# Kernel tuning notes

Measured on AMD Instinct MI355X. Metric: run time of the kernel, lower is better.

The kernel has to match this reference:

```python
import jax, jax.numpy as jnp
import numpy as np


def _igd(x, pf):
    # pf: [M, d] reference front, x: [N, d] candidate set
    # squared Euclidean distances via ||a||^2 + ||b||^2 - 2 a.b (cdist expansion)
    pf_sq = jnp.sum(pf * pf, axis=1, keepdims=True)          # [M, 1]
    x_sq = jnp.sum(x * x, axis=1, keepdims=True).T            # [1, N]
    cross = pf @ x.T                                          # [M, N]
    d2 = jnp.maximum(pf_sq + x_sq - 2.0 * cross, 0.0)
    dist = jnp.sqrt(d2)                                       # [M, N]
    # IGD: mean over reference points of min distance to candidate set
    return jnp.mean(jnp.min(dist, axis=1))


def setup_inputs() -> dict:
    key = jax.random.key(0)
    k1, k2 = jax.random.split(key)
    N, M, D = 16384, 16384, 64
    x = jax.random.normal(k1, (N, D), dtype=jnp.float32)
    pf = jax.random.normal(k2, (M, D), dtype=jnp.float32)
    return {"x": x, "pf": pf}


def reference(x, pf):
    return _igd(x, pf)
```

## Files before the change

kernel.cpp:

```cpp
#include <hip/hip_runtime.h>
#include <hip/hip_bf16.h>


typedef __bf16 bf16x8 __attribute__((ext_vector_type(8)));
typedef float f32x16 __attribute__((ext_vector_type(16)));

#define DIM 64
#define NSPLIT 12
#define MTILE 256

__global__ void pack_kernel(const float* __restrict__ x, const float* __restrict__ pf,
                            __bf16* __restrict__ Bp, __bf16* __restrict__ Ab,
                            float* __restrict__ xsq, float* __restrict__ pfsq,
                            float* __restrict__ out, int N, int M) {
    int gid = blockIdx.x * blockDim.x + threadIdx.x;
    if (gid == 0) out[0] = 0.f;
    if (gid < N * 4) {
        int col = gid >> 2, kf = gid & 3;
        const float* s = x + (size_t)col * DIM + kf * 16;
        float partial = 0.f;
        bf16x8 outv[2];
#pragma unroll
        for (int h = 0; h < 2; ++h) {
            float4 v0 = *(const float4*)(s + h * 8);
            float4 v1 = *(const float4*)(s + h * 8 + 4);
            float f[8] = {v0.x, v0.y, v0.z, v0.w, v1.x, v1.y, v1.z, v1.w};
#pragma unroll
            for (int i = 0; i < 8; ++i) {
                __bf16 b = (__bf16)f[i];
                outv[h][i] = b;
                float bb = (float)b;
                partial += bb * bb;
            }
        }
        int u = col >> 5, c31 = col & 31;
        *(bf16x8*)(Bp + ((size_t)(u * 4 + kf) * 64 + c31) * 8)      = outv[0];
        *(bf16x8*)(Bp + ((size_t)(u * 4 + kf) * 64 + 32 + c31) * 8) = outv[1];
        partial += __shfl_xor(partial, 1);
        partial += __shfl_xor(partial, 2);
        if (kf == 0) xsq[col] = partial;
    } else {
        int g = gid - N * 4;
        int row = g >> 2, q = g & 3;
        if (row >= M) return;
        const float* s = pf + (size_t)row * DIM + q * 16;
        float partial = 0.f;
        bf16x8 outv[2];
#pragma unroll
        for (int h = 0; h < 2; ++h) {
            float4 v0 = *(const float4*)(s + h * 8);
            float4 v1 = *(const float4*)(s + h * 8 + 4);
            float f[8] = {v0.x, v0.y, v0.z, v0.w, v1.x, v1.y, v1.z, v1.w};
#pragma unroll
            for (int i = 0; i < 8; ++i) {
                __bf16 b = (__bf16)(f[i] * -2.f);
                outv[h][i] = b;
                float bb = (float)b;
                partial += bb * bb;
            }
        }
        *(bf16x8*)(Ab + (size_t)row * DIM + q * 16)     = outv[0];
        *(bf16x8*)(Ab + (size_t)row * DIM + q * 16 + 8) = outv[1];
        partial += __shfl_xor(partial, 1);
        partial += __shfl_xor(partial, 2);
        if (q == 0) pfsq[row] = partial * 0.25f;
    }
}

__global__ __launch_bounds__(256, 3)
void igd_main(const __bf16* __restrict__ A, const __bf16* __restrict__ Bp,
              const float* __restrict__ xsq, float* __restrict__ partial, int N) {
    const int mTile  = blockIdx.x;
    const int nsplit = blockIdx.y;
    const int lane = threadIdx.x & 63;
    const int wave = threadIdx.x >> 6;
    const int half = lane >> 5;
    const int l31  = lane & 31;
    const int rowBase = mTile * MTILE + wave * 64;

    const int utotal = N / 32;
    const int ubase  = utotal / NSPLIT;
    const int urem   = utotal % NSPLIT;
    const int ustart = nsplit * ubase + (nsplit < urem ? nsplit : urem);
    const int ucount = ubase + (nsplit < urem ? 1 : 0);

    bf16x8 a[2][4];
#pragma unroll
    for (int g = 0; g < 2; ++g) {
        const __bf16* ap = A + (size_t)(rowBase + 32 * g + l31) * DIM + half * 8;
#pragma unroll
        for (int kf = 0; kf < 4; ++kf)
            a[g][kf] = *(const bf16x8*)(ap + kf * 16);
    }

    f32x16 zero, m0, m1;
#pragma unroll
    for (int r = 0; r < 16; ++r) { zero[r] = 0.f; m0[r] = 1e30f; m1[r] = 1e30f; }

    const __bf16* bbase = Bp + (size_t)ustart * 2048 + (size_t)lane * 8;
    const float*  xbase = xsq + ustart * 32 + l31;

    bf16x8 bA[4], bB[4];
    float xqA, xqB;

#define LOADU(breg, xq, u)                                                     \
    {                                                                          \
        const __bf16* p = bbase + (size_t)(u) * 2048;                          \
        breg[0] = *(const bf16x8*)(p);                                         \
        breg[1] = *(const bf16x8*)(p + 512);                                   \
        breg[2] = *(const bf16x8*)(p + 1024);                                  \
        breg[3] = *(const bf16x8*)(p + 1536);                                  \
        xq = xbase[(u) * 32];                                                  \
    }

#define COMPUTE(breg, xq)                                                      \
    {                                                                          \
        f32x16 acc0 = __builtin_amdgcn_mfma_f32_32x32x16_bf16(a[0][0], breg[0], zero, 0, 0, 0); \
        f32x16 acc1 = __builtin_amdgcn_mfma_f32_32x32x16_bf16(a[1][0], breg[0], zero, 0, 0, 0); \
        _Pragma("unroll")                                                      \
        for (int kf = 1; kf < 4; ++kf) {                                       \
            acc0 = __builtin_amdgcn_mfma_f32_32x32x16_bf16(a[0][kf], breg[kf], acc0, 0, 0, 0); \
            acc1 = __builtin_amdgcn_mfma_f32_32x32x16_bf16(a[1][kf], breg[kf], acc1, 0, 0, 0); \
        }                                                                      \
        _Pragma("unroll")                                                      \
        for (int r = 0; r < 16; ++r) {                                         \
            m0[r] = fminf(m0[r], acc0[r] + xq);                                \
            m1[r] = fminf(m1[r], acc1[r] + xq);                                \
        }                                                                      \
    }

    LOADU(bA, xqA, 0);
    int u = 0;
    for (; u + 2 < ucount; u += 2) {
        LOADU(bB, xqB, u + 1);
        COMPUTE(bA, xqA);
        LOADU(bA, xqA, u + 2);
        COMPUTE(bB, xqB);
    }
    if (u + 1 < ucount) {
        LOADU(bB, xqB, u + 1);
        COMPUTE(bA, xqA);
        COMPUTE(bB, xqB);
    } else {
        COMPUTE(bA, xqA);
    }
#undef LOADU
#undef COMPUTE

#pragma unroll
    for (int mask = 1; mask <= 16; mask <<= 1) {
#pragma unroll
        for (int r = 0; r < 16; ++r) {
            m0[r] = fminf(m0[r], __shfl_xor(m0[r], mask));
            m1[r] = fminf(m1[r], __shfl_xor(m1[r], mask));
        }
    }
    if (l31 == 0) {
#pragma unroll
        for (int r = 0; r < 16; ++r) {
            int row0 = rowBase + (r & 3) + 8 * (r >> 2) + 4 * half;
            partial[(size_t)row0 * NSPLIT + nsplit] = m0[r];
            partial[(size_t)(row0 + 32) * NSPLIT + nsplit] = m1[r];
        }
    }
}

__global__ void reduce_kernel(const float* __restrict__ partial, const float* __restrict__ pfsq,
                              float* __restrict__ out, int M, float invM) {
    int row = blockIdx.x * blockDim.x + threadIdx.x;
    float v = 0.f;
    if (row < M) {
        const float* p = partial + (size_t)row * NSPLIT;
        float mn = 3.4e38f;
#pragma unroll
        for (int s = 0; s < NSPLIT; ++s) mn = fminf(mn, p[s]);
        float d2 = mn + pfsq[row];
        v = sqrtf(fmaxf(d2, 0.f)) * invM;
    }
#pragma unroll
    for (int m = 1; m < 64; m <<= 1) v += __shfl_xor(v, m);
    __shared__ float wsum[4];
    int lane = threadIdx.x & 63, w = threadIdx.x >> 6;
    if (lane == 0) wsum[w] = v;
    __syncthreads();
    if (threadIdx.x == 0) atomicAdd(out, wsum[0] + wsum[1] + wsum[2] + wsum[3]);
}

extern "C" void kernel_launch(void* const* d_in, const int* in_sizes, int n_in,
                              void* d_out, int out_size, void* d_ws, size_t ws_size,
                              hipStream_t stream) {
    const float* x  = (const float*)d_in[0];
    const float* pf = (const float*)d_in[1];
    const int N = in_sizes[0] / DIM;
    const int M = in_sizes[1] / DIM;

    char* ws = (char*)d_ws;
    __bf16* Bp   = (__bf16*)ws;
    __bf16* Ab   = (__bf16*)(ws + (size_t)N * DIM * 2);
    float*  xsq  = (float*)(ws + (size_t)(N + M) * DIM * 2);
    float*  pfsq = xsq + N;
    float*  part = pfsq + M;

    int packThreads = (N + M) * 4;
    pack_kernel<<<dim3((packThreads + 255) / 256), 256, 0, stream>>>(
        x, pf, Bp, Ab, xsq, pfsq, (float*)d_out, N, M);
    igd_main<<<dim3(M / MTILE, NSPLIT), 256, 0, stream>>>(Ab, Bp, xsq, part, N);
    reduce_kernel<<<dim3((M + 255) / 256), 256, 0, stream>>>(part, pfsq, (float*)d_out, M, 1.f / (float)M);
}
```

Baseline: 100.6 us.

## Fold x-norm addition into extra MFMA k-slice via hi/lo bf16 split

```diff
diff --git a/kernel.cpp b/kernel.cpp
--- a/kernel.cpp
+++ b/kernel.cpp
@@ -6,18 +6,19 @@
 typedef float f32x16 __attribute__((ext_vector_type(16)));
 
 #define DIM 64
+#define KF 5
+#define USTRIDE (KF * 64 * 8)
 #define NSPLIT 12
 #define MTILE 256
 
 __global__ void pack_kernel(const float* __restrict__ x, const float* __restrict__ pf,
                             __bf16* __restrict__ Bp, __bf16* __restrict__ Ab,
-                            float* __restrict__ xsq, float* __restrict__ pfsq,
-                            float* __restrict__ out, int N, int M) {
+                            float* __restrict__ pfsq, float* __restrict__ out, int N, int M) {
     int gid = blockIdx.x * blockDim.x + threadIdx.x;
     if (gid == 0) out[0] = 0.f;
     if (gid < N * 4) {
-        int col = gid >> 2, kf = gid & 3;
-        const float* s = x + (size_t)col * DIM + kf * 16;
+        int col = gid >> 2, t = gid & 3;
+        const float* s = x + (size_t)col * DIM + t * 16;
         float partial = 0.f;
         bf16x8 outv[2];
 #pragma unroll
@@ -34,11 +35,21 @@
             }
         }
         int u = col >> 5, c31 = col & 31;
-        *(bf16x8*)(Bp + ((size_t)(u * 4 + kf) * 64 + c31) * 8)      = outv[0];
-        *(bf16x8*)(Bp + ((size_t)(u * 4 + kf) * 64 + 32 + c31) * 8) = outv[1];
+        __bf16* ub = Bp + (size_t)u * USTRIDE;
+        *(bf16x8*)(ub + ((size_t)t * 64 + c31) * 8)      = outv[0];
+        *(bf16x8*)(ub + ((size_t)t * 64 + 32 + c31) * 8) = outv[1];
         partial += __shfl_xor(partial, 1);
         partial += __shfl_xor(partial, 2);
-        if (kf == 0) xsq[col] = partial;
+        if (t == 0) {
+            __bf16 hi = (__bf16)partial;
+            __bf16 lo = (__bf16)(partial - (float)hi);
+            bf16x8 slot0, zero8;
+#pragma unroll
+            for (int i = 0; i < 8; ++i) { slot0[i] = (__bf16)0.f; zero8[i] = (__bf16)0.f; }
+            slot0[0] = hi; slot0[1] = lo;
+            *(bf16x8*)(ub + ((size_t)4 * 64 + c31) * 8)      = slot0;
+            *(bf16x8*)(ub + ((size_t)4 * 64 + 32 + c31) * 8) = zero8;
+        }
     } else {
         int g = gid - N * 4;
         int row = g >> 2, q = g & 3;
@@ -69,7 +80,7 @@
 
 __global__ __launch_bounds__(256, 3)
 void igd_main(const __bf16* __restrict__ A, const __bf16* __restrict__ Bp,
-              const float* __restrict__ xsq, float* __restrict__ partial, int N) {
+              float* __restrict__ partial, int N) {
     const int mTile  = blockIdx.x;
     const int nsplit = blockIdx.y;
     const int lane = threadIdx.x & 63;
@@ -92,28 +103,30 @@
         for (int kf = 0; kf < 4; ++kf)
             a[g][kf] = *(const bf16x8*)(ap + kf * 16);
     }
+    bf16x8 a4;
+#pragma unroll
+    for (int i = 0; i < 8; ++i) a4[i] = (__bf16)0.f;
+    if (half == 0) { a4[0] = (__bf16)1.f; a4[1] = (__bf16)1.f; }
 
     f32x16 zero, m0, m1;
 #pragma unroll
     for (int r = 0; r < 16; ++r) { zero[r] = 0.f; m0[r] = 1e30f; m1[r] = 1e30f; }
 
-    const __bf16* bbase = Bp + (size_t)ustart * 2048 + (size_t)lane * 8;
-    const float*  xbase = xsq + ustart * 32 + l31;
-
-    bf16x8 bA[4], bB[4];
-    float xqA, xqB;
-
-#define LOADU(breg, xq, u)                                                     \
+    const __bf16* bbase = Bp + (size_t)ustart * USTRIDE + (size_t)lane * 8;
+
+    bf16x8 b0[KF], b1[KF];
+
+#define LOADU(breg, u)                                                         \
     {                                                                          \
-        const __bf16* p = bbase + (size_t)(u) * 2048;                          \
+        const __bf16* p = bbase + (size_t)(u) * USTRIDE;                       \
         breg[0] = *(const bf16x8*)(p);                                         \
         breg[1] = *(const bf16x8*)(p + 512);                                   \
         breg[2] = *(const bf16x8*)(p + 1024);                                  \
         breg[3] = *(const bf16x8*)(p + 1536);                                  \
-        xq = xbase[(u) * 32];                                                  \
-    }
-
-#define COMPUTE(breg, xq)                                                      \
+        breg[4] = *(const bf16x8*)(p + 2048);                                  \
+    }
+
+#define COMPUTE(breg)                                                          \
     {                                                                          \
         f32x16 acc0 = __builtin_amdgcn_mfma_f32_32x32x16_bf16(a[0][0], breg[0], zero, 0, 0, 0); \
         f32x16 acc1 = __builtin_amdgcn_mfma_f32_32x32x16_bf16(a[1][0], breg[0], zero, 0, 0, 0); \
@@ -122,28 +135,28 @@
             acc0 = __builtin_amdgcn_mfma_f32_32x32x16_bf16(a[0][kf], breg[kf], acc0, 0, 0, 0); \
             acc1 = __builtin_amdgcn_mfma_f32_32x32x16_bf16(a[1][kf], breg[kf], acc1, 0, 0, 0); \
         }                                                                      \
+        acc0 = __builtin_amdgcn_mfma_f32_32x32x16_bf16(a4, breg[4], acc0, 0, 0, 0); \
+        acc1 = __builtin_amdgcn_mfma_f32_32x32x16_bf16(a4, breg[4], acc1, 0, 0, 0); \
         _Pragma("unroll")                                                      \
         for (int r = 0; r < 16; ++r) {                                         \
-            m0[r] = fminf(m0[r], acc0[r] + xq);                                \
-            m1[r] = fminf(m1[r], acc1[r] + xq);                                \
+            m0[r] = fminf(m0[r], acc0[r]);                                     \
+            m1[r] = fminf(m1[r], acc1[r]);                                     \
         }                                                                      \
     }
 
-    LOADU(bA, xqA, 0);
+    LOADU(b0, 0);
+    LOADU(b1, 1);
     int u = 0;
-    for (; u + 2 < ucount; u += 2) {
-        LOADU(bB, xqB, u + 1);
-        COMPUTE(bA, xqA);
-        LOADU(bA, xqA, u + 2);
-        COMPUTE(bB, xqB);
-    }
-    if (u + 1 < ucount) {
-        LOADU(bB, xqB, u + 1);
-        COMPUTE(bA, xqA);
-        COMPUTE(bB, xqB);
-    } else {
-        COMPUTE(bA, xqA);
-    }
+    for (; u + 3 < ucount; u += 2) {
+        COMPUTE(b0);
+        LOADU(b0, u + 2);
+        COMPUTE(b1);
+        LOADU(b1, u + 3);
+    }
+    COMPUTE(b0);
+    if (u + 2 < ucount) LOADU(b0, u + 2);
+    COMPUTE(b1);
+    if (u + 2 < ucount) COMPUTE(b0);
 #undef LOADU
 #undef COMPUTE
 
@@ -196,14 +209,13 @@
 
     char* ws = (char*)d_ws;
     __bf16* Bp   = (__bf16*)ws;
-    __bf16* Ab   = (__bf16*)(ws + (size_t)N * DIM * 2);
-    float*  xsq  = (float*)(ws + (size_t)(N + M) * DIM * 2);
-    float*  pfsq = xsq + N;
+    __bf16* Ab   = (__bf16*)(ws + (size_t)N * 80 * 2);
+    float*  pfsq = (float*)(ws + (size_t)N * 80 * 2 + (size_t)M * DIM * 2);
     float*  part = pfsq + M;
 
     int packThreads = (N + M) * 4;
     pack_kernel<<<dim3((packThreads + 255) / 256), 256, 0, stream>>>(
-        x, pf, Bp, Ab, xsq, pfsq, (float*)d_out, N, M);
-    igd_main<<<dim3(M / MTILE, NSPLIT), 256, 0, stream>>>(Ab, Bp, xsq, part, N);
+        x, pf, Bp, Ab, pfsq, (float*)d_out, N, M);
+    igd_main<<<dim3(M / MTILE, NSPLIT), 256, 0, stream>>>(Ab, Bp, part, N);
     reduce_kernel<<<dim3((M + 255) / 256), 256, 0, stream>>>(part, pfsq, (float*)d_out, M, 1.f / (float)M);
 }
```

Measured after the change: 109.6 us. +8.9%, slower.

## Switch distance GEMM to FP8 e4m3 MFMA with LDS-staged candidate tiles

Applied to the files above, without the earlier changes.

```diff
diff --git a/kernel.cpp b/kernel.cpp
--- a/kernel.cpp
+++ b/kernel.cpp
@@ -1,66 +1,91 @@
 #include <hip/hip_runtime.h>
-#include <hip/hip_bf16.h>
-
-
-typedef __bf16 bf16x8 __attribute__((ext_vector_type(8)));
+
+
 typedef float f32x16 __attribute__((ext_vector_type(16)));
+typedef unsigned long long u64;
 
 #define DIM 64
-#define NSPLIT 12
+#define NSPLIT 64
+#define UNITS 8
+#define USTRIDE 2048
 #define MTILE 256
 
+__device__ inline unsigned char enc_e4m3(float f) {
+    unsigned int u = __float_as_uint(f);
+    unsigned int s = (u >> 24) & 0x80u;
+    unsigned int a = u & 0x7FFFFFFFu;
+    if ((a >> 23) >= 121u) {
+        unsigned int lsb = (a >> 20) & 1u;
+        unsigned int r = a + 0x7FFFFu + lsb;
+        int e = (int)(r >> 23) - 120;
+        unsigned int m = (r >> 20) & 7u;
+        if (e > 15 || (e == 15 && m == 7u)) return (unsigned char)(s | 0x7Eu);
+        return (unsigned char)(s | ((unsigned)e << 3) | m);
+    }
+    int m = (int)rintf(__uint_as_float(a) * 512.0f);
+    return (unsigned char)(s | (unsigned)m);
+}
+
+__device__ inline float dec_e4m3(unsigned char b) {
+    int e = (b >> 3) & 15, m = b & 7;
+    float v = (e == 0) ? (float)m * 0.001953125f
+                       : (float)(8 + m) * exp2f((float)(e - 10));
+    return (b & 0x80) ? -v : v;
+}
+
 __global__ void pack_kernel(const float* __restrict__ x, const float* __restrict__ pf,
-                            __bf16* __restrict__ Bp, __bf16* __restrict__ Ab,
+                            unsigned char* __restrict__ Bp, unsigned char* __restrict__ Ab,
                             float* __restrict__ xsq, float* __restrict__ pfsq,
                             float* __restrict__ out, int N, int M) {
     int gid = blockIdx.x * blockDim.x + threadIdx.x;
     if (gid == 0) out[0] = 0.f;
     if (gid < N * 4) {
-        int col = gid >> 2, kf = gid & 3;
-        const float* s = x + (size_t)col * DIM + kf * 16;
+        int col = gid >> 2, t = gid & 3;
+        const float* s = x + (size_t)col * DIM + t * 16;
         float partial = 0.f;
-        bf16x8 outv[2];
+        u64 w[2] = {0, 0};
 #pragma unroll
         for (int h = 0; h < 2; ++h) {
             float4 v0 = *(const float4*)(s + h * 8);
             float4 v1 = *(const float4*)(s + h * 8 + 4);
             float f[8] = {v0.x, v0.y, v0.z, v0.w, v1.x, v1.y, v1.z, v1.w};
 #pragma unroll
-            for (int i = 0; i < 8; ++i) {
-                __bf16 b = (__bf16)f[i];
-                outv[h][i] = b;
-                float bb = (float)b;
-                partial += bb * bb;
+            for (int j = 0; j < 8; ++j) {
+                unsigned char b = enc_e4m3(f[j]);
+                w[h] |= (u64)b << (8 * j);
+                float d = dec_e4m3(b);
+                partial += d * d;
             }
         }
         int u = col >> 5, c31 = col & 31;
-        *(bf16x8*)(Bp + ((size_t)(u * 4 + kf) * 64 + c31) * 8)      = outv[0];
-        *(bf16x8*)(Bp + ((size_t)(u * 4 + kf) * 64 + 32 + c31) * 8) = outv[1];
+        unsigned char* ub = Bp + (size_t)u * USTRIDE + (size_t)t * 512;
+        *(u64*)(ub + (size_t)c31 * 8)        = w[0];
+        *(u64*)(ub + (size_t)(32 + c31) * 8) = w[1];
         partial += __shfl_xor(partial, 1);
         partial += __shfl_xor(partial, 2);
-        if (kf == 0) xsq[col] = partial;
+        if (t == 0) xsq[col] = partial;
     } else {
         int g = gid - N * 4;
         int row = g >> 2, q = g & 3;
         if (row >= M) return;
         const float* s = pf + (size_t)row * DIM + q * 16;
         float partial = 0.f;
-        bf16x8 outv[2];
+        u64 w[2] = {0, 0};
 #pragma unroll
         for (int h = 0; h < 2; ++h) {
             float4 v0 = *(const float4*)(s + h * 8);
             float4 v1 = *(const float4*)(s + h * 8 + 4);
             float f[8] = {v0.x, v0.y, v0.z, v0.w, v1.x, v1.y, v1.z, v1.w};
 #pragma unroll
-            for (int i = 0; i < 8; ++i) {
-                __bf16 b = (__bf16)(f[i] * -2.f);
-                outv[h][i] = b;
-                float bb = (float)b;
-                partial += bb * bb;
+            for (int j = 0; j < 8; ++j) {
+                unsigned char b = enc_e4m3(f[j] * -2.f);
+                w[h] |= (u64)b << (8 * j);
+                float d = dec_e4m3(b);
+                partial += d * d;
             }
         }
-        *(bf16x8*)(Ab + (size_t)row * DIM + q * 16)     = outv[0];
-        *(bf16x8*)(Ab + (size_t)row * DIM + q * 16 + 8) = outv[1];
+        *(u64*)(Ab + (size_t)row * DIM + q * 16)     = w[0];
+        *(u64*)(Ab + (size_t)row * DIM + q * 16 + 8) = w[1];
         partial += __shfl_xor(partial, 1);
         partial += __shfl_xor(partial, 2);
         if (q == 0) pfsq[row] = partial * 0.25f;
@@ -68,59 +93,64 @@
 }
 
 __global__ __launch_bounds__(256, 3)
-void igd_main(const __bf16* __restrict__ A, const __bf16* __restrict__ Bp,
-              const float* __restrict__ xsq, float* __restrict__ partial, int N) {
+void igd_main(const unsigned char* __restrict__ A, const unsigned char* __restrict__ Bp,
+              const float* __restrict__ xsq, float* __restrict__ partial) {
+    __shared__ unsigned char ldsB[UNITS * USTRIDE];
+    __shared__ float ldsX[UNITS * 32];
+    const int tid = threadIdx.x;
     const int mTile  = blockIdx.x;
     const int nsplit = blockIdx.y;
-    const int lane = threadIdx.x & 63;
-    const int wave = threadIdx.x >> 6;
+    const int lane = tid & 63;
+    const int wave = tid >> 6;
     const int half = lane >> 5;
     const int l31  = lane & 31;
     const int rowBase = mTile * MTILE + wave * 64;
 
-    const int utotal = N / 32;
-    const int ubase  = utotal / NSPLIT;
-    const int urem   = utotal % NSPLIT;
-    const int ustart = nsplit * ubase + (nsplit < urem ? nsplit : urem);
-    const int ucount = ubase + (nsplit < urem ? 1 : 0);
-
-    bf16x8 a[2][4];
+    u64 a[2][4];
 #pragma unroll
     for (int g = 0; g < 2; ++g) {
-        const __bf16* ap = A + (size_t)(rowBase + 32 * g + l31) * DIM + half * 8;
+        const unsigned char* ap = A + (size_t)(rowBase + 32 * g + l31) * DIM + half * 8;
 #pragma unroll
         for (int kf = 0; kf < 4; ++kf)
-            a[g][kf] = *(const bf16x8*)(ap + kf * 16);
-    }
+            a[g][kf] = *(const u64*)(ap + kf * 16);
+    }
+
+    {
+        const char* gsrc = (const char*)Bp + (size_t)nsplit * (UNITS * USTRIDE);
+#pragma unroll
+        for (int i = 0; i < 4; ++i)
+            *(float4*)(ldsB + i * 4096 + tid * 16) = *(const float4*)(gsrc + i * 4096 + tid * 16);
+        ldsX[tid] = xsq[nsplit * (UNITS * 32) + tid];
+    }
+    __syncthreads();
 
     f32x16 zero, m0, m1;
 #pragma unroll
     for (int r = 0; r < 16; ++r) { zero[r] = 0.f; m0[r] = 1e30f; m1[r] = 1e30f; }
 
-    const __bf16* bbase = Bp + (size_t)ustart * 2048 + (size_t)lane * 8;
-    const float*  xbase = xsq + ustart * 32 + l31;
-
-    bf16x8 bA[4], bB[4];
+    u64 b0[4], b1[4];
     float xqA, xqB;
 
 #define LOADU(breg, xq, u)                                                     \
     {                                                                          \
-        const __bf16* p = bbase + (size_t)(u) * 2048;                          \
-        breg[0] = *(const bf16x8*)(p);                                         \
-        breg[1] = *(const bf16x8*)(p + 512);                                   \
-        breg[2] = *(const bf16x8*)(p + 1024);                                  \
-        breg[3] = *(const bf16x8*)(p + 1536);                                  \
-        xq = xbase[(u) * 32];                                                  \
+        const unsigned char* p = ldsB + (u) * USTRIDE + lane * 8;              \
+        breg[0] = *(const u64*)(p);                                            \
+        breg[1] = *(const u64*)(p + 512);                                      \
+        breg[2] = *(const u64*)(p + 1024);                                     \
+        breg[3] = *(const u64*)(p + 1536);                                     \
+        xq = ldsX[(u) * 32 + l31];                                             \
     }
 
 #define COMPUTE(breg, xq)                                                      \
     {                                                                          \
-        f32x16 acc0 = __builtin_amdgcn_mfma_f32_32x32x16_bf16(a[0][0], breg[0], zero, 0, 0, 0); \
-        f32x16 acc1 = __builtin_amdgcn_mfma_f32_32x32x16_bf16(a[1][0], breg[0], zero, 0, 0, 0); \
+        f32x16 acc0 = __builtin_amdgcn_mfma_f32_32x32x16_fp8_fp8((long)breg[0], (long)breg[0], zero, 0, 0, 0); \
+        acc0 = zero;                                                           \
+        acc0 = __builtin_amdgcn_mfma_f32_32x32x16_fp8_fp8((long)a[0][0], (long)breg[0], zero, 0, 0, 0); \
+        f32x16 acc1 = __builtin_amdgcn_mfma_f32_32x32x16_fp8_fp8((long)a[1][0], (long)breg[0], zero, 0, 0, 0); \
         _Pragma("unroll")                                                      \
         for (int kf = 1; kf < 4; ++kf) {                                       \
-            acc0 = __builtin_amdgcn_mfma_f32_32x32x16_bf16(a[0][kf], breg[kf], acc0, 0, 0, 0); \
-            acc1 = __builtin_amdgcn_mfma_f32_32x32x16_bf16(a[1][kf], breg[kf], acc1, 0, 0, 0); \
+            acc0 = __builtin_amdgcn_mfma_f32_32x32x16_fp8_fp8((long)a[0][kf], (long)breg[kf], acc0, 0, 0, 0); \
+            acc1 = __builtin_amdgcn_mfma_f32_32x32x16_fp8_fp8((long)a[1][kf], (long)breg[kf], acc1, 0, 0, 0); \
         }                                                                      \
         _Pragma("unroll")                                                      \
         for (int r = 0; r < 16; ++r) {                                         \
@@ -129,20 +159,13 @@
         }                                                                      \
     }
 
-    LOADU(bA, xqA, 0);
-    int u = 0;
-    for (; u + 2 < ucount; u += 2) {
-        LOADU(bB, xqB, u + 1);
-        COMPUTE(bA, xqA);
-        LOADU(bA, xqA, u + 2);
-        COMPUTE(bB, xqB);
-    }
-    if (u + 1 < ucount) {
-        LOADU(bB, xqB, u + 1);
-        COMPUTE(bA, xqA);
-        COMPUTE(bB, xqB);
-    } else {
-        COMPUTE(bA, xqA);
+    LOADU(b0, xqA, 0);
+#pragma unroll
+    for (int u = 0; u < UNITS; u += 2) {
+        LOADU(b1, xqB, u + 1);
+        COMPUTE(b0, xqA);
+        if (u + 2 < UNITS) LOADU(b0, xqA, u + 2);
+        COMPUTE(b1, xqB);
     }
 #undef LOADU
 #undef COMPUTE
@@ -172,7 +195,7 @@
     if (row < M) {
         const float* p = partial + (size_t)row * NSPLIT;
         float mn = 3.4e38f;
-#pragma unroll
+#pragma unroll 8
         for (int s = 0; s < NSPLIT; ++s) mn = fminf(mn, p[s]);
         float d2 = mn + pfsq[row];
         v = sqrtf(fmaxf(d2, 0.f)) * invM;
@@ -195,15 +218,15 @@
     const int M = in_sizes[1] / DIM;
 
     char* ws = (char*)d_ws;
-    __bf16* Bp   = (__bf16*)ws;
-    __bf16* Ab   = (__bf16*)(ws + (size_t)N * DIM * 2);
-    float*  xsq  = (float*)(ws + (size_t)(N + M) * DIM * 2);
-    float*  pfsq = xsq + N;
-    float*  part = pfsq + M;
+    unsigned char* Bp = (unsigned char*)ws;
+    unsigned char* Ab = (unsigned char*)(ws + (size_t)N * DIM);
+    float* xsq  = (float*)(ws + (size_t)(N + M) * DIM);
+    float* pfsq = xsq + N;
+    float* part = pfsq + M;
 
     int packThreads = (N + M) * 4;
     pack_kernel<<<dim3((packThreads + 255) / 256), 256, 0, stream>>>(
         x, pf, Bp, Ab, xsq, pfsq, (float*)d_out, N, M);
-    igd_main<<<dim3(M / MTILE, NSPLIT), 256, 0, stream>>>(Ab, Bp, xsq, part, N);
+    igd_main<<<dim3(M / MTILE, NSPLIT), 256, 0, stream>>>(Ab, Bp, xsq, part);
     reduce_kernel<<<dim3((M + 255) / 256), 256, 0, stream>>>(part, pfsq, (float*)d_out, M, 1.f / (float)M);
 }
```

After: 127.1 us. 26.3% more time.
